# Kernel tuning notes

Measured on AMD Instinct MI355X. Metric: run time of the kernel, lower is better.

## Reference

```python
import jax, jax.numpy as jnp
import numpy as np

B, S, D, H, SPAN = 4, 1024, 768, 12, 512
HD = D // H  # 64


def setup_inputs() -> dict:
    key = jax.random.key(0)
    ks = jax.random.split(key, 8)
    hidden_states = jax.random.normal(ks[0], (B, S, D), jnp.float32)
    rel_embeddings = jax.random.normal(ks[1], (2 * SPAN, D), jnp.float32) * 0.02
    Wq = jax.random.normal(ks[2], (D, D), jnp.float32) * 0.02
    Wk = jax.random.normal(ks[3], (D, D), jnp.float32) * 0.02
    Wv = jax.random.normal(ks[4], (D, D), jnp.float32) * 0.02
    Wo = jax.random.normal(ks[5], (D, D), jnp.float32) * 0.02
    bq = jnp.zeros((D,), jnp.float32); bk = jnp.zeros((D,), jnp.float32)
    bv = jnp.zeros((D,), jnp.float32); bo = jnp.zeros((D,), jnp.float32)
    ln_g = jnp.ones((D,), jnp.float32); ln_b = jnp.zeros((D,), jnp.float32)
    idx = jnp.arange(S)
    relative_pos = (idx[:, None] - idx[None, :]).astype(jnp.int32)  # q - k
    lengths = jnp.array([1024, 896, 768, 512])  # padding-style mask
    valid = idx[None, :] < lengths[:, None]  # [B,S]
    attention_mask = (valid[:, :, None] & valid[:, None, :])[:, None, :, :].astype(jnp.int32)  # [B,1,S,S]
    return dict(hidden_states=hidden_states, rel_embeddings=rel_embeddings,
                Wq=Wq, bq=bq, Wk=Wk, bk=bk, Wv=Wv, bv=bv, Wo=Wo, bo=bo,
                ln_g=ln_g, ln_b=ln_b, attention_mask=attention_mask,
                relative_pos=relative_pos)


def reference(hidden_states, rel_embeddings, Wq, bq, Wk, bk, Wv, bv, Wo, bo,
              ln_g, ln_b, attention_mask, relative_pos):
    # content projections -> [B,H,S,HD]
    q = (hidden_states @ Wq.T + bq).reshape(B, S, H, HD).transpose(0, 2, 1, 3)
    k = (hidden_states @ Wk.T + bk).reshape(B, S, H, HD).transpose(0, 2, 1, 3)
    v = (hidden_states @ Wv.T + bv).reshape(B, S, H, HD).transpose(0, 2, 1, 3)

    scale_qk = jnp.sqrt(jnp.float32(HD * 3))  # scale_factor = 3
    scores = jnp.einsum('bhqd,bhkd->bhqk', q, k) / scale_qk

    # shared-key position projections -> [H, 2*SPAN, HD]
    pos_q = (rel_embeddings @ Wq.T + bq).reshape(2 * SPAN, H, HD).transpose(1, 0, 2)
    pos_k = (rel_embeddings @ Wk.T + bk).reshape(2 * SPAN, H, HD).transpose(1, 0, 2)

    rp = relative_pos.astype(jnp.int32)
    # c2p: query vs relative key-position embedding, gathered by clamp(rel+span)
    c2p_att = jnp.einsum('bhqd,hkd->bhqk', q, pos_k)  # [B,H,S,2*SPAN]
    c2p_pos = jnp.clip(rp + SPAN, 0, 2 * SPAN - 1)
    c2p_idx = jnp.broadcast_to(c2p_pos[None, None], (B, H, S, S))
    c2p = jnp.take_along_axis(c2p_att, c2p_idx, axis=-1) / scale_qk

    # p2c: key vs relative query-position embedding, gathered by clamp(-rel+span), then transposed
    p2c_att = jnp.einsum('bhkd,hqd->bhkq', k, pos_q)  # [B,H,S,2*SPAN]
    p2c_pos = jnp.clip(SPAN - rp, 0, 2 * SPAN - 1)
    p2c_idx = jnp.broadcast_to(p2c_pos[None, None], (B, H, S, S))
    p2c = jnp.swapaxes(jnp.take_along_axis(p2c_att, p2c_idx, axis=-1), -1, -2)
    p2c = p2c / jnp.sqrt(jnp.float32(HD))  # note: torch uses sqrt(d) here, no scale_factor

    scores = scores + c2p + p2c

    # XSoftmax: masked softmax with zeros at masked positions
    mask = attention_mask.astype(bool)  # [B,1,S,S]
    neg = jnp.finfo(scores.dtype).min
    probs = jax.nn.softmax(jnp.where(mask, scores, neg), axis=-1)
    probs = jnp.where(mask, probs, jnp.float32(0))

    ctx = jnp.einsum('bhqk,bhkd->bhqd', probs, v).transpose(0, 2, 1, 3).reshape(B, S, D)

    # DebertaV2SelfOutput: dense + residual + LayerNorm(eps=1e-7)
    x = ctx @ Wo.T + bo + hidden_states
    mu = x.mean(-1, keepdims=True)
    var = ((x - mu) ** 2).mean(-1, keepdims=True)
    return (x - mu) / jnp.sqrt(var + 1e-7) * ln_g + ln_b
```

## Files before the change

kernel.cpp:

```cpp
#include <hip/hip_runtime.h>
#include <hip/hip_bf16.h>
#include <stdint.h>

typedef __hip_bfloat16 bf16;
typedef __attribute__((ext_vector_type(8))) short s8v;
typedef __attribute__((ext_vector_type(4))) float f4v;

__device__ __align__(16) bf16 g_hidden[4096 * 768];
__device__ __align__(16) bf16 g_rel[1024 * 768];
__device__ __align__(16) bf16 g_Wqkv[2304 * 768];
__device__ __align__(16) bf16 g_Wo[768 * 768];
__device__ __align__(16) bf16 g_biasQKV[2304];
__device__ __align__(16) bf16 g_biasPos[1536];
__device__ __align__(16) bf16 g_bo[768];
__device__ __align__(16) bf16 g_lng[768];
__device__ __align__(16) bf16 g_lnb[768];
__device__ __align__(16) bf16 g_Y1[4096 * 1536];
__device__ __align__(16) bf16 g_VT[48u * 64 * 1024];
__device__ __align__(16) bf16 g_Yp[1024 * 1536];
__device__ __align__(16) bf16 g_ctx[4096 * 768];
__device__ __align__(16) float g_X[4096 * 768];
__device__ int g_vq[4096], g_vk[4096], g_kmax[4];

__device__ __forceinline__ float bfs(short x) {
  return __uint_as_float(((unsigned int)(unsigned short)x) << 16);
}
__device__ __forceinline__ unsigned short f2bf(float f) {
  bf16 h = __float2bfloat16(f);
  return *(unsigned short*)&h;
}
__device__ __forceinline__ bool detect_bf16(const void* lng_raw) {
  return *(const unsigned int*)lng_raw == 0x3F803F80u;
}

__device__ __forceinline__ void cvt4(const void* src, bf16* dst, long grp, bool isbf) {
  long e = grp * 4;
  if (isbf) {
    *(uint2*)(dst + e) = *(const uint2*)((const bf16*)src + e);
  } else {
    float4 f = *(const float4*)((const float*)src + e);
    union { unsigned short us[4]; uint2 v; } u;
    u.us[0] = f2bf(f.x); u.us[1] = f2bf(f.y); u.us[2] = f2bf(f.z); u.us[3] = f2bf(f.w);
    *(uint2*)(dst + e) = u.v;
  }
}

__global__ __launch_bounds__(256) void cvt_inputs(
    const void* h, const void* r,
    const void* wq, const void* wk, const void* wv, const void* wo,
    const void* bq, const void* bk, const void* bv, const void* bo,
    const void* lg, const void* lb)
{
  if (blockIdx.x == 0 && threadIdx.x < 4) g_kmax[threadIdx.x] = 0;
  const bool isbf = detect_bf16(lg);
  long i = (long)blockIdx.x * 256 + threadIdx.x;
  if (i < 786432) { cvt4(h,  g_hidden,          i, isbf); return; } i -= 786432;
  if (i < 196608) { cvt4(r,  g_rel,             i, isbf); return; } i -= 196608;
  if (i < 147456) { cvt4(wq, g_Wqkv,            i, isbf); return; } i -= 147456;
  if (i < 147456) { cvt4(wk, g_Wqkv + 589824,   i, isbf); return; } i -= 147456;
  if (i < 147456) { cvt4(wv, g_Wqkv + 1179648,  i, isbf); return; } i -= 147456;
  if (i < 147456) { cvt4(wo, g_Wo,              i, isbf); return; } i -= 147456;
  if (i < 192)    { cvt4(bq, g_biasQKV,         i, isbf); return; } i -= 192;
  if (i < 192)    { cvt4(bk, g_biasQKV + 768,   i, isbf); return; } i -= 192;
  if (i < 192)    { cvt4(bv, g_biasQKV + 1536,  i, isbf); return; } i -= 192;
  if (i < 192)    { cvt4(bq, g_biasPos,         i, isbf); return; } i -= 192;
  if (i < 192)    { cvt4(bk, g_biasPos + 768,   i, isbf); return; } i -= 192;
  if (i < 192)    { cvt4(lg, g_lng,             i, isbf); return; } i -= 192;
  if (i < 192)    { cvt4(lb, g_lnb,             i, isbf); return; }
}

__global__ __launch_bounds__(256) void mask_prep(const int* __restrict__ mask) {
  int t = blockIdx.x * 256 + threadIdx.x;
  int b = t >> 10, i = t & 1023;
  int vq = mask[((size_t)(b * 1024 + i)) * 1024];
  int vk = mask[((size_t)(b * 1024)) * 1024 + i];
  g_vq[t] = vq;
  g_vk[t] = vk;
  if (vq | vk) atomicMax(&g_kmax[b], i + 1);
}

__global__ __launch_bounds__(256, 2) void gemm_bt(int which) {
  __shared__ short As[128][72];
  __shared__ short Bs[128][72];

  const bf16 *A, *B; const bf16* bias;
  int lda, ldb, K, mode;
  const int m0 = blockIdx.y * 128, n0 = blockIdx.x * 128;

  if (which == 0) {
    A = g_hidden; lda = 768; B = g_Wqkv; ldb = 768; bias = g_biasQKV; K = 768;
    mode = (n0 >= 1536) ? 5 : 0;
  } else if (which == 1) {
    A = g_rel; lda = 768; B = g_Wqkv; ldb = 768; bias = g_biasPos; K = 768; mode = 1;
  } else {
    A = g_ctx; lda = 768; B = g_Wo; ldb = 768; bias = g_bo; K = 768; mode = 4;
  }

  const int tid = threadIdx.x, wave = tid >> 6, lane = tid & 63;
  const int quad = lane >> 4, l15 = lane & 15;
  const int wm = (wave >> 1) * 64, wn = (wave & 1) * 64;
  const int sr = tid >> 2, sc8 = (tid & 3) * 16;

  f4v acc[4][4];
#pragma unroll
  for (int i = 0; i < 4; i++)
#pragma unroll
    for (int j = 0; j < 4; j++) acc[i][j] = (f4v){0.f, 0.f, 0.f, 0.f};

  uint4 pa0, pa1, pa2, pa3, pb0, pb1, pb2, pb3;
#define LOAD_T(k0)                                                           \
  {                                                                          \
    const bf16* ap = A + (size_t)(m0 + sr) * lda + (k0) + sc8;               \
    const bf16* ap2 = A + (size_t)(m0 + sr + 64) * lda + (k0) + sc8;         \
    const bf16* bp = B + (size_t)(n0 + sr) * ldb + (k0) + sc8;               \
    const bf16* bp2 = B + (size_t)(n0 + sr + 64) * ldb + (k0) + sc8;         \
    pa0 = *(const uint4*)ap;  pa1 = *(const uint4*)(ap + 8);                 \
    pa2 = *(const uint4*)ap2; pa3 = *(const uint4*)(ap2 + 8);                \
    pb0 = *(const uint4*)bp;  pb1 = *(const uint4*)(bp + 8);                 \
    pb2 = *(const uint4*)bp2; pb3 = *(const uint4*)(bp2 + 8);                \
  }

  LOAD_T(0)
  for (int k0 = 0; k0 < K; k0 += 64) {
    __syncthreads();
    *(uint4*)&As[sr][sc8] = pa0;      *(uint4*)&As[sr][sc8 + 8] = pa1;
    *(uint4*)&As[sr + 64][sc8] = pa2; *(uint4*)&As[sr + 64][sc8 + 8] = pa3;
    *(uint4*)&Bs[sr][sc8] = pb0;      *(uint4*)&Bs[sr][sc8 + 8] = pb1;
    *(uint4*)&Bs[sr + 64][sc8] = pb2; *(uint4*)&Bs[sr + 64][sc8 + 8] = pb3;
    if (k0 + 64 < K) LOAD_T(k0 + 64)
    __syncthreads();

    s8v af[4][2], bfr[4][2];
#pragma unroll
    for (int mt = 0; mt < 4; mt++) {
      af[mt][0] = *(const s8v*)&As[wm + mt * 16 + l15][quad * 8];
      af[mt][1] = *(const s8v*)&As[wm + mt * 16 + l15][32 + quad * 8];
    }
#pragma unroll
    for (int nt = 0; nt < 4; nt++) {
      bfr[nt][0] = *(const s8v*)&Bs[wn + nt * 16 + l15][quad * 8];
      bfr[nt][1] = *(const s8v*)&Bs[wn + nt * 16 + l15][32 + quad * 8];
    }
#pragma unroll
    for (int mt = 0; mt < 4; mt++)
#pragma unroll
      for (int nt = 0; nt < 4; nt++) {
        acc[mt][nt] = __builtin_amdgcn_mfma_f32_16x16x32_bf16(af[mt][0], bfr[nt][0], acc[mt][nt], 0, 0, 0);
        acc[mt][nt] = __builtin_amdgcn_mfma_f32_16x16x32_bf16(af[mt][1], bfr[nt][1], acc[mt][nt], 0, 0, 0);
      }
  }
#undef LOAD_T

  float biasv[4];
#pragma unroll
  for (int nt = 0; nt < 4; nt++)
    biasv[nt] = bfs(*(const short*)&bias[n0 + wn + nt * 16 + l15]);

#pragma unroll
  for (int mt = 0; mt < 4; mt++) {
#pragma unroll
    for (int nt = 0; nt < 4; nt++) {
      const int mbase = m0 + wm + mt * 16 + quad * 4;
      const int n = n0 + wn + nt * 16 + l15;
      if (mode == 5) {
        const int dd = n - 1536, hv = dd >> 6, hd = dd & 63;
        const int bb = mbase >> 10, ss = mbase & 1023;
        float t0 = acc[mt][nt][0] + biasv[nt], t1 = acc[mt][nt][1] + biasv[nt];
        float t2 = acc[mt][nt][2] + biasv[nt], t3 = acc[mt][nt][3] + biasv[nt];
        uint2 pk;
        pk.x = (unsigned int)f2bf(t0) | ((unsigned int)f2bf(t1) << 16);
        pk.y = (unsigned int)f2bf(t2) | ((unsigned int)f2bf(t3) << 16);
        *(uint2*)(g_VT + (((size_t)(bb * 12 + hv) * 64 + hd) << 10) + ss) = pk;
        continue;
      }
#pragma unroll
      for (int reg = 0; reg < 4; reg++) {
        const int m = mbase + reg;
        float v = acc[mt][nt][reg] + biasv[nt];
        if (mode == 0) {
          g_Y1[(size_t)m * 1536 + n] = __float2bfloat16(v);
        } else if (mode == 1) {
          g_Yp[(size_t)m * 1536 + n] = __float2bfloat16(v);
        } else {
          v += bfs(*(const short*)&g_hidden[(size_t)m * 768 + n]);
          g_X[(size_t)m * 768 + n] = v;
        }
      }
    }
  }
}

__global__ __launch_bounds__(256, 3) void attn_mfma() {
  const int bh = blockIdx.y, b = bh / 12, hh = bh - b * 12;
  const int q0 = blockIdx.x * 64;
  const int tid = threadIdx.x, wave = tid >> 6, lane = tid & 63;
  const int quad = lane >> 4, l15 = lane & 15;
  const int kmax = g_kmax[b];

  if (q0 >= kmax) {
    uint4 zz = {0u, 0u, 0u, 0u};
#pragma unroll
    for (int s = tid; s < 512; s += 256) {
      int r = s >> 3, cc = (s & 7) * 8;
      *(uint4*)(g_ctx + (size_t)(b * 1024 + q0 + r) * 768 + hh * 64 + cc) = zz;
    }
    return;
  }

  __shared__ short BandPK[128][72];
  __shared__ short BandPQ[128][72];
  __shared__ short Pl[4][16][72];
  short* C2Pr = &BandPK[0][0];
  short* P2Cr = &BandPQ[0][0];

  const size_t qrow = (size_t)(b * 1024 + q0 + wave * 16 + l15) * 1536 + hh * 64;
  const s8v qf0 = *(const s8v*)(g_Y1 + qrow + quad * 8);
  const s8v qf1 = *(const s8v*)(g_Y1 + qrow + 32 + quad * 8);

  int vqr[4];
#pragma unroll
  for (int reg = 0; reg < 4; reg++)
    vqr[reg] = g_vq[b * 1024 + q0 + wave * 16 + quad * 4 + reg];

  f4v accO[4];
#pragma unroll
  for (int dt = 0; dt < 4; dt++) accO[dt] = (f4v){0.f, 0.f, 0.f, 0.f};
  float psum[4] = {0.f, 0.f, 0.f, 0.f};

  const bf16* Kbase = g_Y1 + (size_t)(b * 1024) * 1536 + 768 + hh * 64;
  const bf16* Vbase = g_VT + ((size_t)bh << 16);
  const bf16* PKbase = g_Yp + 768 + hh * 64;
  const bf16* PQbase = g_Yp + hh * 64;

  const int brow = tid >> 1, bcol = (tid & 1) * 32;
  uint4 rpk[4], rpq[4];
#define LOAD_B(k0)                                                          \
  {                                                                         \
    int jk = min(max(q0 - (k0) + 449 + brow, 0), 1023);                     \
    const bf16* pk = PKbase + (size_t)jk * 1536 + bcol;                     \
    rpk[0] = *(const uint4*)pk;        rpk[1] = *(const uint4*)(pk + 8);    \
    rpk[2] = *(const uint4*)(pk + 16); rpk[3] = *(const uint4*)(pk + 24);   \
    int jq = min(max((k0) - q0 + 449 + brow, 0), 1023);                     \
    const bf16* pq = PQbase + (size_t)jq * 1536 + bcol;                     \
    rpq[0] = *(const uint4*)pq;        rpq[1] = *(const uint4*)(pq + 8);    \
    rpq[2] = *(const uint4*)(pq + 16); rpq[3] = *(const uint4*)(pq + 24);   \
  }

  LOAD_B(0)
  const float r192 = 0.0721687836487032f;
  const float r64 = 0.125f;

  for (int k0 = 0; k0 < kmax; k0 += 64) {
    __syncthreads();
    *(uint4*)&BandPK[brow][bcol] = rpk[0];      *(uint4*)&BandPK[brow][bcol + 8] = rpk[1];
    *(uint4*)&BandPK[brow][bcol + 16] = rpk[2]; *(uint4*)&BandPK[brow][bcol + 24] = rpk[3];
    *(uint4*)&BandPQ[brow][bcol] = rpq[0];      *(uint4*)&BandPQ[brow][bcol + 8] = rpq[1];
    *(uint4*)&BandPQ[brow][bcol + 16] = rpq[2]; *(uint4*)&BandPQ[brow][bcol + 24] = rpq[3];
    if (k0 + 64 < kmax) LOAD_B(k0 + 64)
    __syncthreads();

    const bf16* karow = Kbase + (size_t)(k0 + wave * 16 + l15) * 1536;
    const s8v ka0 = *(const s8v*)(karow + quad * 8);
    const s8v ka1 = *(const s8v*)(karow + 32 + quad * 8);

    f4v sacc[4];
#pragma unroll
    for (int nt = 0; nt < 4; nt++) {
      const bf16* kbrow = Kbase + (size_t)(k0 + nt * 16 + l15) * 1536;
      s8v kb0 = *(const s8v*)(kbrow + quad * 8);
      s8v kb1 = *(const s8v*)(kbrow + 32 + quad * 8);
      sacc[nt] = __builtin_amdgcn_mfma_f32_16x16x32_bf16(qf0, kb0, (f4v){0.f, 0.f, 0.f, 0.f}, 0, 0, 0);
      sacc[nt] = __builtin_amdgcn_mfma_f32_16x16x32_bf16(qf1, kb1, sacc[nt], 0, 0, 0);
    }

    f4v cacc[5], pacc[5];
#pragma unroll
    for (int t2 = 0; t2 < 5; t2++) {
      const int nr = (wave + t2) * 16 + l15;
      s8v b0 = *(const s8v*)&BandPK[nr][quad * 8];
      s8v b1 = *(const s8v*)&BandPK[nr][32 + quad * 8];
      cacc[t2] = __builtin_amdgcn_mfma_f32_16x16x32_bf16(qf0, b0, (f4v){0.f, 0.f, 0.f, 0.f}, 0, 0, 0);
      cacc[t2] = __builtin_amdgcn_mfma_f32_16x16x32_bf16(qf1, b1, cacc[t2], 0, 0, 0);
      s8v c0 = *(const s8v*)&BandPQ[nr][quad * 8];
      s8v c1 = *(const s8v*)&BandPQ[nr][32 + quad * 8];
      pacc[t2] = __builtin_amdgcn_mfma_f32_16x16x32_bf16(ka0, c0, (f4v){0.f, 0.f, 0.f, 0.f}, 0, 0, 0);
      pacc[t2] = __builtin_amdgcn_mfma_f32_16x16x32_bf16(ka1, c1, pacc[t2], 0, 0, 0);
    }

    __syncthreads();
#pragma unroll
    for (int t2 = 0; t2 < 5; t2++) {
      const int col = t2 * 16 + l15;
#pragma unroll
      for (int reg = 0; reg < 4; reg++) {
        const int row = wave * 16 + quad * 4 + reg;
        C2Pr[row * 88 + col] = (short)f2bf(cacc[t2][reg]);
        P2Cr[row * 88 + col] = (short)f2bf(pacc[t2][reg]);
      }
    }
    __syncthreads();

    const bool tail = (k0 + 64 > kmax);
#pragma unroll
    for (int nt = 0; nt < 4; nt++) {
      const int kl = nt * 16 + l15;
#pragma unroll
      for (int reg = 0; reg < 4; reg++) {
        const int qr = quad * 4 + reg;
        float c2 = bfs(C2Pr[(wave * 16 + qr) * 88 + qr - kl + 63]);
        float p2 = bfs(P2Cr[kl * 88 + l15 - wave * 16 - qr + 63]);
        float sc = (sacc[nt][reg] + c2) * r192 + p2 * r64;
        float pe = __expf(fminf(sc, 60.f));
        if (tail && (k0 + kl >= kmax)) pe = 0.f;
        psum[reg] += pe;
        Pl[wave][qr][kl] = (short)f2bf(pe);
      }
    }

    s8v pa0 = *(const s8v*)&Pl[wave][l15][quad * 8];
    s8v pa1 = *(const s8v*)&Pl[wave][l15][32 + quad * 8];
#pragma unroll
    for (int dt = 0; dt < 4; dt++) {
      const bf16* vrow = Vbase + ((size_t)(dt * 16 + l15) << 10) + k0;
      s8v vb0 = *(const s8v*)(vrow + quad * 8);
      s8v vb1 = *(const s8v*)(vrow + 32 + quad * 8);
      accO[dt] = __builtin_amdgcn_mfma_f32_16x16x32_bf16(pa0, vb0, accO[dt], 0, 0, 0);
      accO[dt] = __builtin_amdgcn_mfma_f32_16x16x32_bf16(pa1, vb1, accO[dt], 0, 0, 0);
    }
  }
#undef LOAD_B

#pragma unroll
  for (int off = 1; off < 16; off <<= 1)
#pragma unroll
    for (int reg = 0; reg < 4; reg++) psum[reg] += __shfl_xor(psum[reg], off);

  float inv[4];
#pragma unroll
  for (int reg = 0; reg < 4; reg++)
    inv[reg] = (vqr[reg] != 0 && psum[reg] > 0.f) ? 1.f / psum[reg] : 0.f;

#pragma unroll
  for (int dt = 0; dt < 4; dt++)
#pragma unroll
    for (int reg = 0; reg < 4; reg++) {
      float v = accO[dt][reg] * inv[reg];
      g_ctx[(size_t)(b * 1024 + q0 + wave * 16 + quad * 4 + reg) * 768 + hh * 64 + dt * 16 + l15] =
          __float2bfloat16(v);
    }
}

__global__ __launch_bounds__(256) void ln_kernel(const void* lng_raw, void* out) {
  const bool isbf = detect_bf16(lng_raw);
  const int row = blockIdx.x;
  const int tid = threadIdx.x;
  const float* xr = g_X + (size_t)row * 768;
  float x0 = xr[tid], x1 = xr[tid + 256], x2 = xr[tid + 512];
  float s = x0 + x1 + x2;
  float s2 = x0 * x0 + x1 * x1 + x2 * x2;
#pragma unroll
  for (int off = 32; off; off >>= 1) { s += __shfl_xor(s, off); s2 += __shfl_xor(s2, off); }
  __shared__ float red[2][4];
  int w = tid >> 6, ln = tid & 63;
  if (ln == 0) { red[0][w] = s; red[1][w] = s2; }
  __syncthreads();
  float ts = red[0][0] + red[0][1] + red[0][2] + red[0][3];
  float ts2 = red[1][0] + red[1][1] + red[1][2] + red[1][3];
  float mu = ts * (1.f / 768.f);
  float var = fmaxf(ts2 * (1.f / 768.f) - mu * mu, 0.f);
  float rstd = rsqrtf(var + 1e-7f);
#pragma unroll
  for (int q = 0; q < 3; q++) {
    int cidx = tid + q * 256;
    float xv = (q == 0) ? x0 : (q == 1 ? x1 : x2);
    float gg = bfs(*(const short*)&g_lng[cidx]);
    float bb = bfs(*(const short*)&g_lnb[cidx]);
    float val = (xv - mu) * rstd * gg + bb;
    if (isbf) ((bf16*)out)[(size_t)row * 768 + cidx] = __float2bfloat16(val);
    else      ((float*)out)[(size_t)row * 768 + cidx] = val;
  }
}

extern "C" void kernel_launch(void* const* d_in, const int* in_sizes, int n_in,
                              void* d_out, int out_size, void* d_ws, size_t ws_size,
                              hipStream_t stream) {
  const int* amask = (const int*)d_in[12];
  (void)d_ws; (void)ws_size; (void)in_sizes; (void)n_in; (void)out_size;

  cvt_inputs<<<dim3(6150), 256, 0, stream>>>(
      d_in[0], d_in[1], d_in[2], d_in[4], d_in[6], d_in[8],
      d_in[3], d_in[5], d_in[7], d_in[9], d_in[10], d_in[11]);
  mask_prep<<<dim3(16), 256, 0, stream>>>(amask);
  gemm_bt<<<dim3(18, 32, 1), 256, 0, stream>>>(0);
  gemm_bt<<<dim3(12, 8, 1), 256, 0, stream>>>(1);
  attn_mfma<<<dim3(16, 48), 256, 0, stream>>>();
  gemm_bt<<<dim3(6, 32, 1), 256, 0, stream>>>(4);
  ln_kernel<<<dim3(4096), 256, 0, stream>>>(d_in[10], d_out);
}
```

Before: 440.5 us.

## Read position bands directly from global memory instead of staging in LDS

Drops the register-prefetched LDS staging of the PK/PQ position-embedding bands. Each wave now loads its band rows straight from global memory before its MFMAs and writes c2p/p2c results into separate smaller LDS buffers with a 90-element row stride, which removes one barrier pair per iteration. Launch bounds drop from 3 to 2 blocks per CU. The catch is more redundant global/L2 traffic, since waves overlap on band rows and the old software prefetch is gone, and possibly lower occupancy.

```diff
diff --git a/kernel.cpp b/kernel.cpp
--- a/kernel.cpp
+++ b/kernel.cpp
@@ -190,7 +190,7 @@
   }
 }
 
-__global__ __launch_bounds__(256, 3) void attn_mfma() {
+__global__ __launch_bounds__(256, 2) void attn_mfma() {
   const int bh = blockIdx.y, b = bh / 12, hh = bh - b * 12;
   const int q0 = blockIdx.x * 64;
   const int tid = threadIdx.x, wave = tid >> 6, lane = tid & 63;
@@ -207,11 +207,9 @@
     return;
   }
 
-  __shared__ short BandPK[128][72];
-  __shared__ short BandPQ[128][72];
+  __shared__ short C2Pr[64 * 90];
+  __shared__ short P2Cr[64 * 90];
   __shared__ short Pl[4][16][72];
-  short* C2Pr = &BandPK[0][0];
-  short* P2Cr = &BandPQ[0][0];
 
   const size_t qrow = (size_t)(b * 1024 + q0 + wave * 16 + l15) * 1536 + hh * 64;
   const s8v qf0 = *(const s8v*)(g_Y1 + qrow + quad * 8);
@@ -232,37 +230,10 @@
   const bf16* PKbase = g_Yp + 768 + hh * 64;
   const bf16* PQbase = g_Yp + hh * 64;
 
-  const int brow = tid >> 1, bcol = (tid & 1) * 32;
-  uint4 rpk[4], rpq[4];
-#define LOAD_B(k0)                                                          \
-  {                                                                         \
-    int jk = min(max(q0 - (k0) + 449 + brow, 0), 1023);                     \
-    const bf16* pk = PKbase + (size_t)jk * 1536 + bcol;                     \
-    rpk[0] = *(const uint4*)pk;        rpk[1] = *(const uint4*)(pk + 8);    \
-    rpk[2] = *(const uint4*)(pk + 16); rpk[3] = *(const uint4*)(pk + 24);   \
-    int jq = min(max((k0) - q0 + 449 + brow, 0), 1023);                     \
-    const bf16* pq = PQbase + (size_t)jq * 1536 + bcol;                     \
-    rpq[0] = *(const uint4*)pq;        rpq[1] = *(const uint4*)(pq + 8);    \
-    rpq[2] = *(const uint4*)(pq + 16); rpq[3] = *(const uint4*)(pq + 24);   \
-  }
-
-  LOAD_B(0)
   const float r192 = 0.0721687836487032f;
   const float r64 = 0.125f;
 
   for (int k0 = 0; k0 < kmax; k0 += 64) {
-    __syncthreads();
-    *(uint4*)&BandPK[brow][bcol] = rpk[0];      *(uint4*)&BandPK[brow][bcol + 8] = rpk[1];
-    *(uint4*)&BandPK[brow][bcol + 16] = rpk[2]; *(uint4*)&BandPK[brow][bcol + 24] = rpk[3];
-    *(uint4*)&BandPQ[brow][bcol] = rpq[0];      *(uint4*)&BandPQ[brow][bcol + 8] = rpq[1];
-    *(uint4*)&BandPQ[brow][bcol + 16] = rpq[2]; *(uint4*)&BandPQ[brow][bcol + 24] = rpq[3];
-    if (k0 + 64 < kmax) LOAD_B(k0 + 64)
-    __syncthreads();
-
-    const bf16* karow = Kbase + (size_t)(k0 + wave * 16 + l15) * 1536;
-    const s8v ka0 = *(const s8v*)(karow + quad * 8);
-    const s8v ka1 = *(const s8v*)(karow + 32 + quad * 8);
-
     f4v sacc[4];
 #pragma unroll
     for (int nt = 0; nt < 4; nt++) {
@@ -272,30 +243,34 @@
       sacc[nt] = __builtin_amdgcn_mfma_f32_16x16x32_bf16(qf0, kb0, (f4v){0.f, 0.f, 0.f, 0.f}, 0, 0, 0);
       sacc[nt] = __builtin_amdgcn_mfma_f32_16x16x32_bf16(qf1, kb1, sacc[nt], 0, 0, 0);
     }
-
-    f4v cacc[5], pacc[5];
+    const bf16* karow = Kbase + (size_t)(k0 + wave * 16 + l15) * 1536;
+    const s8v ka0 = *(const s8v*)(karow + quad * 8);
+    const s8v ka1 = *(const s8v*)(karow + 32 + quad * 8);
+
+    __syncthreads();
+
+    const int cbase = q0 - k0 + 449, pbase = k0 - q0 + 449;
 #pragma unroll
     for (int t2 = 0; t2 < 5; t2++) {
       const int nr = (wave + t2) * 16 + l15;
-      s8v b0 = *(const s8v*)&BandPK[nr][quad * 8];
-      s8v b1 = *(const s8v*)&BandPK[nr][32 + quad * 8];
-      cacc[t2] = __builtin_amdgcn_mfma_f32_16x16x32_bf16(qf0, b0, (f4v){0.f, 0.f, 0.f, 0.f}, 0, 0, 0);
-      cacc[t2] = __builtin_amdgcn_mfma_f32_16x16x32_bf16(qf1, b1, cacc[t2], 0, 0, 0);
-      s8v c0 = *(const s8v*)&BandPQ[nr][quad * 8];
-      s8v c1 = *(const s8v*)&BandPQ[nr][32 + quad * 8];
-      pacc[t2] = __builtin_amdgcn_mfma_f32_16x16x32_bf16(ka0, c0, (f4v){0.f, 0.f, 0.f, 0.f}, 0, 0, 0);
-      pacc[t2] = __builtin_amdgcn_mfma_f32_16x16x32_bf16(ka1, c1, pacc[t2], 0, 0, 0);
-    }
-
-    __syncthreads();
-#pragma unroll
-    for (int t2 = 0; t2 < 5; t2++) {
+      int jk = min(max(cbase + nr, 0), 1023);
+      const bf16* pkrow = PKbase + (size_t)jk * 1536;
+      s8v b0 = *(const s8v*)(pkrow + quad * 8);
+      s8v b1 = *(const s8v*)(pkrow + 32 + quad * 8);
+      f4v cacc = __builtin_amdgcn_mfma_f32_16x16x32_bf16(qf0, b0, (f4v){0.f, 0.f, 0.f, 0.f}, 0, 0, 0);
+      cacc = __builtin_amdgcn_mfma_f32_16x16x32_bf16(qf1, b1, cacc, 0, 0, 0);
+      int jq = min(max(pbase + nr, 0), 1023);
+      const bf16* pqrow = PQbase + (size_t)jq * 1536;
+      s8v c0 = *(const s8v*)(pqrow + quad * 8);
+      s8v c1 = *(const s8v*)(pqrow + 32 + quad * 8);
+      f4v pacc = __builtin_amdgcn_mfma_f32_16x16x32_bf16(ka0, c0, (f4v){0.f, 0.f, 0.f, 0.f}, 0, 0, 0);
+      pacc = __builtin_amdgcn_mfma_f32_16x16x32_bf16(ka1, c1, pacc, 0, 0, 0);
       const int col = t2 * 16 + l15;
 #pragma unroll
       for (int reg = 0; reg < 4; reg++) {
         const int row = wave * 16 + quad * 4 + reg;
-        C2Pr[row * 88 + col] = (short)f2bf(cacc[t2][reg]);
-        P2Cr[row * 88 + col] = (short)f2bf(pacc[t2][reg]);
+        C2Pr[row * 90 + col] = (short)f2bf(cacc[reg]);
+        P2Cr[row * 90 + col] = (short)f2bf(pacc[reg]);
       }
     }
     __syncthreads();
@@ -307,8 +282,8 @@
 #pragma unroll
       for (int reg = 0; reg < 4; reg++) {
         const int qr = quad * 4 + reg;
-        float c2 = bfs(C2Pr[(wave * 16 + qr) * 88 + qr - kl + 63]);
-        float p2 = bfs(P2Cr[kl * 88 + l15 - wave * 16 - qr + 63]);
+        float c2 = bfs(C2Pr[(wave * 16 + qr) * 90 + qr - kl + 63]);
+        float p2 = bfs(P2Cr[kl * 90 + l15 - wave * 16 - qr + 63]);
         float sc = (sacc[nt][reg] + c2) * r192 + p2 * r64;
         float pe = __expf(fminf(sc, 60.f));
         if (tail && (k0 + kl >= kmax)) pe = 0.f;
@@ -328,7 +303,6 @@
       accO[dt] = __builtin_amdgcn_mfma_f32_16x16x32_bf16(pa1, vb1, accO[dt], 0, 0, 0);
     }
   }
-#undef LOAD_B
 
 #pragma unroll
   for (int off = 1; off < 16; off <<= 1)
```

Result: faster. 417.6 us (-5.2%).
